# Optimization experiments

Hardware: AMD Instinct MI355X
Metric: run time of the kernel (lower is better)

The kernel has to match this reference:

```python
import jax, jax.numpy as jnp
import numpy as np

EPS = 1e-5

def _conv3x3(x, w, b):
    y = jax.lax.conv_general_dilated(x, w, window_strides=(1, 1),
                                     padding=((1, 1), (1, 1)),
                                     dimension_numbers=('NCHW', 'OIHW', 'NCHW'))
    return y + b[None, :, None, None]

def _bilinear_gather(x, py, px):
    # x: [B,C,H,W]; py,px: [B,K,H,W] absolute sampling coords; zero outside image (DCN convention).
    B, C, H, W = x.shape
    Kk = py.shape[1]
    y0 = jnp.floor(py)
    x0 = jnp.floor(px)
    ly = py - y0
    lx = px - x0
    y0i = y0.astype(jnp.int32)
    x0i = x0.astype(jnp.int32)
    xf = x.reshape(B, C, H * W)

    def gather(yi, xi):
        valid = (yi >= 0) & (yi < H) & (xi >= 0) & (xi < W)
        idx = (jnp.clip(yi, 0, H - 1) * W + jnp.clip(xi, 0, W - 1)).reshape(B, -1)
        g = jax.vmap(lambda xb, ib: xb[:, ib])(xf, idx).reshape(B, C, Kk, H, W)
        return g * valid[:, None].astype(x.dtype)

    v00 = gather(y0i, x0i)
    v01 = gather(y0i, x0i + 1)
    v10 = gather(y0i + 1, x0i)
    v11 = gather(y0i + 1, x0i + 1)
    ly = ly[:, None]
    lx = lx[:, None]
    return (v00 * (1 - ly) * (1 - lx) + v01 * (1 - ly) * lx
            + v10 * ly * (1 - lx) + v11 * ly * lx)

def _shift_forward(x, w_off, b_off, w_conv, b_conv, gamma, beta, run_mean, run_var):
    B, C, H, W = x.shape
    om = _conv3x3(x, w_off, b_off)              # [B,27,H,W] offset/mask predictor
    dy = om[:, 0:18:2]                          # [B,9,H,W] per-tap y offsets
    dx = om[:, 1:18:2]                          # [B,9,H,W] per-tap x offsets
    mask = jax.nn.sigmoid(om[:, 18:27])         # [B,9,H,W] modulation (DCNv2)
    kk = jnp.arange(3, dtype=x.dtype) - 1.0     # kernel tap offsets for 3x3, dilation 1
    ky = jnp.repeat(kk, 3)                      # [9]
    kx = jnp.tile(kk, 3)                        # [9]
    hh = jnp.arange(H, dtype=x.dtype)
    ww = jnp.arange(W, dtype=x.dtype)
    py = hh[None, None, :, None] + ky[None, :, None, None] + dy
    px = ww[None, None, None, :] + kx[None, :, None, None] + dx
    s = _bilinear_gather(x, py, px) * mask[:, None]   # [B,C,9,H,W]
    Co = w_conv.shape[0]
    y = jnp.einsum('bckhw,ock->bohw', s, w_conv.reshape(Co, C, 9))
    y = y + b_conv[None, :, None, None]
    # BatchNorm2d (inference) + ReLU, then residual add
    inv = jax.lax.rsqrt(run_var + EPS)
    y = (y - run_mean[None, :, None, None]) * (inv * gamma)[None, :, None, None] + beta[None, :, None, None]
    y = jax.nn.relu(y)
    return x + y

def setup_inputs():
    key = jax.random.key(0)
    ks = jax.random.split(key, 3)
    B, C, H, W = 2, 256, 96, 96
    x = jax.random.normal(ks[0], (B, C, H, W), dtype=jnp.float32)
    w_off = jax.random.normal(ks[1], (27, C, 3, 3), dtype=jnp.float32) * 0.01
    b_off = jnp.zeros((27,), dtype=jnp.float32)
    w_conv = jax.random.normal(ks[2], (C, C, 3, 3), dtype=jnp.float32) * 0.02
    b_conv = jnp.zeros((C,), dtype=jnp.float32)
    gamma = jnp.ones((C,), dtype=jnp.float32)
    beta = jnp.zeros((C,), dtype=jnp.float32)
    run_mean = jnp.zeros((C,), dtype=jnp.float32)
    run_var = jnp.ones((C,), dtype=jnp.float32)
    return {"x": x, "w_off": w_off, "b_off": b_off, "w_conv": w_conv,
            "b_conv": b_conv, "gamma": gamma, "beta": beta,
            "run_mean": run_mean, "run_var": run_var}

def reference(x, w_off, b_off, w_conv, b_conv, gamma, beta, run_mean, run_var):
    return _shift_forward(x, w_off, b_off, w_conv, b_conv, gamma, beta, run_mean, run_var)
```

## Files before the change

kernel.cpp:

```cpp
#include <hip/hip_runtime.h>
#include <hip/hip_bf16.h>

#define H_ 96
#define W_ 96
#define HW_ 9216
#define C_ 256
#define B_ 2
#define KO_ 27
#define NPX_ 18432
#define EPS_ 1e-5f

typedef unsigned short u16;
typedef unsigned short ushort8 __attribute__((ext_vector_type(8)));
typedef unsigned short ushort4v __attribute__((ext_vector_type(4)));
typedef short short8v __attribute__((ext_vector_type(8)));
typedef float float4v __attribute__((ext_vector_type(4)));

__device__ __forceinline__ float b2f(u16 u) {
    return __uint_as_float(((unsigned int)u) << 16);
}
__device__ __forceinline__ u16 f2b(float f) {
    __hip_bfloat16 h = __float2bfloat16(f);
    union { __hip_bfloat16 h; u16 u; } cv; cv.h = h; return cv.u;
}
__device__ __forceinline__ unsigned int pack2(float a, float b) {
    union { __hip_bfloat162 h; unsigned int u; } cv;
    cv.h = __float22bfloat162_rn(make_float2(a, b));
    return cv.u;
}

__global__ __launch_bounds__(256) void prep_kernel(
    const float* __restrict__ x,
    const float* __restrict__ w_conv, const float* __restrict__ w_off,
    const float* __restrict__ b_conv,
    const float* __restrict__ gamma, const float* __restrict__ beta,
    const float* __restrict__ rmean, const float* __restrict__ rvar,
    float* __restrict__ AB, u16* __restrict__ WQ, u16* __restrict__ WO,
    u16* __restrict__ XT)
{
    __shared__ u16 ls[32][100];
    const int bx = blockIdx.x;
    if (bx < 2304) {
        if (bx == 0) {
            int o = threadIdx.x;
            float sc = gamma[o] * rsqrtf(rvar[o] + EPS_);
            AB[o] = sc;
            AB[256 + o] = beta[o] + (b_conv[o] - rmean[o]) * sc;
        }
        int idx = bx * 256 + threadIdx.x;
        int ch = idx >> 13;
        int o  = (idx >> 5) & 255;
        int cp = idx & 31;
        int c  = ((ch & 7) << 5) + cp;
        int k  = ch >> 3;
        WQ[idx] = f2b(w_conv[(o * C_ + c) * 9 + k]);
    } else if (bx < 2592) {
        int j = (bx - 2304) * 256 + threadIdx.x;
        int ch = j >> 10;
        int o  = (j >> 5) & 31;
        int cp = j & 31;
        int c  = ((ch & 7) << 5) + cp;
        int k  = ch >> 3;
        WO[j] = (o < KO_) ? f2b(w_off[(o * C_ + c) * 9 + k]) : (u16)0;
    } else {
        int bid = bx - 2592;
        int h  = bid % 96;
        int by = bid / 96;
        int cg = by & 7;
        int b  = by >> 3;
        int c0 = cg * 32;
        for (int e = threadIdx.x; e < 32 * W_; e += 256) {
            int ci = e / W_, w = e % W_;
            ls[ci][w] = f2b(x[((b * C_ + c0 + ci) * H_ + h) * W_ + w]);
        }
        __syncthreads();
        for (int u = threadIdx.x; u < 768; u += 256) {
            int g4 = u & 7, w = u >> 3;
            ushort4v v;
#pragma unroll
            for (int t = 0; t < 4; t++) v[t] = ls[g4 * 4 + t][w];
            *(ushort4v*)&XT[((b * H_ + h) * W_ + w) * C_ + c0 + g4 * 4] = v;
        }
    }
}

__global__ __launch_bounds__(256) void fused_kernel(
    const float* __restrict__ x, const u16* __restrict__ XT,
    const u16* __restrict__ WO, const float* __restrict__ b_off,
    const u16* __restrict__ WQ, const float* __restrict__ AB,
    float* __restrict__ out)
{
    __shared__ float red[4][2][32][17];
    __shared__ __align__(16) u16 sB[2048];
    __shared__ float offv[32][36];

    const int tid  = threadIdx.x;
    const int wave = tid >> 6;
    const int lane = tid & 63;
    const int quad = lane >> 4;
    const int l15  = lane & 15;

    const int bid = blockIdx.x;
    const int swz = (bid & 7) * 72 + (bid >> 3);
    const int n0  = swz * 32;
    const int b   = n0 / HW_;
    const int p0  = n0 - b * HW_;
    const int h   = p0 / W_;
    const int w0  = p0 % W_;

    {
        float4v oa[2][2];
#pragma unroll
        for (int ph = 0; ph < 2; ph++)
#pragma unroll
            for (int hh = 0; hh < 2; hh++)
                oa[ph][hh] = float4v{0.f, 0.f, 0.f, 0.f};

        int basec0 = 0, basec1 = 0; bool vld0 = true, vld1 = true;
        auto oset = [&](int tap) {
            int py = h + tap / 3 - 1;
            bool vy = (unsigned)py < (unsigned)H_;
            int pyc = min(max(py, 0), H_ - 1);
            int rowb = (b * H_ + pyc) * W_;
            {
                int pxl = w0 + l15 + tap % 3 - 1;
                vld0 = vy && ((unsigned)pxl < (unsigned)W_);
                basec0 = (rowb + min(max(pxl, 0), W_ - 1)) * C_ + quad * 8;
            }
            {
                int pxl = w0 + 16 + l15 + tap % 3 - 1;
                vld1 = vy && ((unsigned)pxl < (unsigned)W_);
                basec1 = (rowb + min(max(pxl, 0), W_ - 1)) * C_ + quad * 8;
            }
        };
        auto bld0 = [&](int c32) -> ushort8 {
            ushort8 v = *(const ushort8*)(XT + basec0 + (c32 & 7) * 32);
#pragma unroll
            for (int j = 0; j < 8; j++) v[j] = vld0 ? v[j] : (u16)0;
            return v;
        };
        auto bld1 = [&](int c32) -> ushort8 {
            ushort8 v = *(const ushort8*)(XT + basec1 + (c32 & 7) * 32);
#pragma unroll
            for (int j = 0; j < 8; j++) v[j] = vld1 ? v[j] : (u16)0;
            return v;
        };
        const int i0 = wave * 18, i1 = i0 + 18;
        int curtap = i0 >> 3;
        oset(curtap);
        ushort8 b0 = bld0(i0), b1 = bld1(i0);
        short8v wa = *(const short8v*)(WO + i0 * 1024 + l15 * 32 + quad * 8);
        short8v wb = *(const short8v*)(WO + i0 * 1024 + l15 * 32 + quad * 8 + 512);
        for (int i = i0; i < i1; ++i) {
            ushort8 c0v = b0, c1v = b1;
            short8v wac = wa, wbc = wb;
            int nx = i + 1;
            if (nx < i1) {
                int t = nx >> 3;
                if (t != curtap) { oset(t); curtap = t; }
                b0 = bld0(nx); b1 = bld1(nx);
                wa = *(const short8v*)(WO + nx * 1024 + l15 * 32 + quad * 8);
                wb = *(const short8v*)(WO + nx * 1024 + l15 * 32 + quad * 8 + 512);
            }
            union { ushort8 u; short8v s; } u0, u1; u0.u = c0v; u1.u = c1v;
            oa[0][0] = __builtin_amdgcn_mfma_f32_16x16x32_bf16(wac, u0.s, oa[0][0], 0, 0, 0);
            oa[0][1] = __builtin_amdgcn_mfma_f32_16x16x32_bf16(wbc, u0.s, oa[0][1], 0, 0, 0);
            oa[1][0] = __builtin_amdgcn_mfma_f32_16x16x32_bf16(wac, u1.s, oa[1][0], 0, 0, 0);
            oa[1][1] = __builtin_amdgcn_mfma_f32_16x16x32_bf16(wbc, u1.s, oa[1][1], 0, 0, 0);
        }
#pragma unroll
        for (int r = 0; r < 4; ++r) {
            red[wave][0][quad * 4 + r][l15]      = oa[0][0][r];
            red[wave][0][16 + quad * 4 + r][l15] = oa[0][1][r];
            red[wave][1][quad * 4 + r][l15]      = oa[1][0][r];
            red[wave][1][16 + quad * 4 + r][l15] = oa[1][1][r];
        }
    }
    __syncthreads();
    for (int u = tid; u < 1024; u += 256) {
        int px = u & 31, o = u >> 5;
        if (o < KO_) {
            int ph = px >> 4, pp = px & 15;
            float v = red[0][ph][o][pp] + red[1][ph][o][pp]
                    + red[2][ph][o][pp] + red[3][ph][o][pp] + b_off[o];
            offv[px][o] = (o < 18) ? v : 1.f / (1.f + expf(-v));
        }
    }
    __syncthreads();

    float4v acc[4][2];
#pragma unroll
    for (int i = 0; i < 4; i++)
#pragma unroll
        for (int jj = 0; jj < 2; jj++)
            acc[i][jj] = float4v{0.f, 0.f, 0.f, 0.f};

    const int wo  = wave * 64;
    const int ppx = tid >> 3;
    const int pj  = tid & 7;
    const int sboff = (pj >> 2) * 1024 + ppx * 32 + (((pj & 3) ^ (ppx & 3)) << 3);
    const int bslot = (quad ^ (l15 & 3)) << 3;

    float fc0, fc1, fc2, fc3, fn0, fn1, fn2, fn3;
    int a00, a01, a10, a11;

    auto tap_setup = [&](int tap) {
        float dy = offv[ppx][2 * tap];
        float dx = offv[ppx][2 * tap + 1];
        float m  = offv[ppx][18 + tap];
        float py  = (float)(h + tap / 3 - 1) + dy;
        float pxx = (float)(w0 + ppx + tap % 3 - 1) + dx;
        float y0f = floorf(py), x0f = floorf(pxx);
        float ly = py - y0f, lx = pxx - x0f;
        int y0 = (int)y0f, x0i = (int)x0f;
        int y1 = y0 + 1, x1 = x0i + 1;
        bool vy0 = (unsigned)y0 < (unsigned)H_;
        bool vy1 = (unsigned)y1 < (unsigned)H_;
        bool vx0 = (unsigned)x0i < (unsigned)W_;
        bool vx1 = (unsigned)x1 < (unsigned)W_;
        fn0 = (vy0 && vx0) ? (1.f - ly) * (1.f - lx) * m : 0.f;
        fn1 = (vy0 && vx1) ? (1.f - ly) * lx * m : 0.f;
        fn2 = (vy1 && vx0) ? ly * (1.f - lx) * m : 0.f;
        fn3 = (vy1 && vx1) ? ly * lx * m : 0.f;
        int y0c = min(max(y0, 0), H_ - 1), y1c = min(max(y1, 0), H_ - 1);
        int x0c = min(max(x0i, 0), W_ - 1), x1c = min(max(x1, 0), W_ - 1);
        a00 = ((b * H_ + y0c) * W_ + x0c) * C_;
        a01 = ((b * H_ + y0c) * W_ + x1c) * C_;
        a10 = ((b * H_ + y1c) * W_ + x0c) * C_;
        a11 = ((b * H_ + y1c) * W_ + x1c) * C_;
    };

    tap_setup(0);
    fc0 = fn0; fc1 = fn1; fc2 = fn2; fc3 = fn3;
    ushort8 gc00 = *(const ushort8*)(XT + a00 + pj * 8);
    ushort8 gc01 = *(const ushort8*)(XT + a01 + pj * 8);
    ushort8 gc10 = *(const ushort8*)(XT + a10 + pj * 8);
    ushort8 gc11 = *(const ushort8*)(XT + a11 + pj * 8);
    ushort8 gn00{}, gn01{}, gn10{}, gn11{};

#pragma unroll 1
    for (int ch = 0; ch < 36; ++ch) {
        const int tap = ch >> 2, q = ch & 3;

        short8v af[2][4];
        const u16* wq0 = WQ + (size_t)(tap * 8 + q * 2) * 8192
                       + (wo + l15) * 32 + quad * 8;
#pragma unroll
        for (int cc = 0; cc < 2; ++cc)
#pragma unroll
            for (int mt = 0; mt < 4; ++mt)
                af[cc][mt] = *(const short8v*)(wq0 + cc * 8192 + mt * 512);

        {
            float v[8];
#pragma unroll
            for (int t = 0; t < 8; t++)
                v[t] = fc0 * b2f(gc00[t]) + fc1 * b2f(gc01[t])
                     + fc2 * b2f(gc10[t]) + fc3 * b2f(gc11[t]);
            uint4 sv;
            sv.x = pack2(v[0], v[1]);
            sv.y = pack2(v[2], v[3]);
            sv.z = pack2(v[4], v[5]);
            sv.w = pack2(v[6], v[7]);
            *(uint4*)&sB[sboff] = sv;
        }

        if (ch < 35) {
            const int chn = ch + 1, tapn = chn >> 2, qn = chn & 3;
            if (qn == 0) tap_setup(tapn);
            const int cb = qn * 64 + pj * 8;
            gn00 = *(const ushort8*)(XT + a00 + cb);
            gn01 = *(const ushort8*)(XT + a01 + cb);
            gn10 = *(const ushort8*)(XT + a10 + cb);
            gn11 = *(const ushort8*)(XT + a11 + cb);
        }

        asm volatile("s_waitcnt lgkmcnt(0)" ::: "memory");
        __builtin_amdgcn_s_barrier();

        short8v bfr[2][2];
#pragma unroll
        for (int cc = 0; cc < 2; ++cc)
#pragma unroll
            for (int nt = 0; nt < 2; ++nt)
                bfr[cc][nt] = *(const short8v*)
                    &sB[cc * 1024 + (nt * 16 + l15) * 32 + bslot];

        asm volatile("s_waitcnt lgkmcnt(0)" ::: "memory");
        __builtin_amdgcn_s_barrier();
        __builtin_amdgcn_sched_barrier(0);

        __builtin_amdgcn_s_setprio(1);
#pragma unroll
        for (int cc = 0; cc < 2; ++cc)
#pragma unroll
            for (int mt = 0; mt < 4; ++mt)
#pragma unroll
                for (int nt = 0; nt < 2; ++nt)
                    acc[mt][nt] = __builtin_amdgcn_mfma_f32_16x16x32_bf16(
                        af[cc][mt], bfr[cc][nt], acc[mt][nt], 0, 0, 0);
        __builtin_amdgcn_s_setprio(0);

        gc00 = gn00; gc01 = gn01; gc10 = gn10; gc11 = gn11;
        fc0 = fn0; fc1 = fn1; fc2 = fn2; fc3 = fn3;
    }

    const float* Ao = AB;
    const float* Bo = AB + 256;
#pragma unroll
    for (int mt = 0; mt < 4; mt++) {
#pragma unroll
        for (int nt = 0; nt < 2; nt++) {
            int pix = p0 + nt * 16 + l15;
#pragma unroll
            for (int r = 0; r < 4; r++) {
                int o = wo + mt * 16 + quad * 4 + r;
                float v = acc[mt][nt][r] * Ao[o] + Bo[o];
                v = fmaxf(v, 0.f);
                int gi = (b * C_ + o) * HW_ + pix;
                out[gi] = x[gi] + v;
            }
        }
    }
}

extern "C" void kernel_launch(void* const* d_in, const int* in_sizes, int n_in,
                              void* d_out, int out_size, void* d_ws, size_t ws_size,
                              hipStream_t stream)
{
    (void)in_sizes; (void)n_in; (void)out_size; (void)ws_size;
    const float* x      = (const float*)d_in[0];
    const float* w_off  = (const float*)d_in[1];
    const float* b_off  = (const float*)d_in[2];
    const float* w_conv = (const float*)d_in[3];
    const float* b_conv = (const float*)d_in[4];
    const float* gamma  = (const float*)d_in[5];
    const float* beta   = (const float*)d_in[6];
    const float* rmean  = (const float*)d_in[7];
    const float* rvar   = (const float*)d_in[8];
    float* out = (float*)d_out;

    float* ws = (float*)d_ws;
    float* AB = ws;
    u16* WQ = (u16*)(AB + 512);
    u16* WO = WQ + 589824;
    u16* XT = WO + 73728;

    prep_kernel<<<4128, 256, 0, stream>>>(x, w_conv, w_off, b_conv, gamma, beta,
                                          rmean, rvar, AB, WQ, WO, XT);
    fused_kernel<<<576, 256, 0, stream>>>(x, XT, WO, b_off, WQ, AB, out);
}
```

Baseline: 175.0 us.

## Split output channels across two blocks and stage weights via async LDS loads

Each block now computes 128 output channels for its 32 pixels, so the grid grows to 1152 blocks. The A-side weight tiles are double-buffered in LDS with global_load_lds, and the prep kernel stores them in a swizzled layout so the LDS reads avoid bank conflicts. The sampled B tile is also double-buffered, with XT prefetched two chunks ahead. The aim is better occupancy across the CUs and less stall on per-wave global weight loads. In exchange, each output-channel half recomputes the offset conv and the bilinear sampling, and the kernel uses more LDS per block.

Measured after the change: 184.7 us. +5.6%, slower.

```diff
diff --git a/kernel.cpp b/kernel.cpp
--- a/kernel.cpp
+++ b/kernel.cpp
@@ -5,9 +5,7 @@
 #define W_ 96
 #define HW_ 9216
 #define C_ 256
-#define B_ 2
 #define KO_ 27
-#define NPX_ 18432
 #define EPS_ 1e-5f
 
 typedef unsigned short u16;
@@ -27,6 +25,11 @@
     union { __hip_bfloat162 h; unsigned int u; } cv;
     cv.h = __float22bfloat162_rn(make_float2(a, b));
     return cv.u;
+}
+__device__ __forceinline__ void glds16(const u16* g, u16* l) {
+    __builtin_amdgcn_global_load_lds(
+        (const __attribute__((address_space(1))) void*)g,
+        (__attribute__((address_space(3))) void*)l, 16, 0, 0);
 }
 
 __global__ __launch_bounds__(256) void prep_kernel(
@@ -50,7 +53,8 @@
         int idx = bx * 256 + threadIdx.x;
         int ch = idx >> 13;
         int o  = (idx >> 5) & 255;
-        int cp = idx & 31;
+        int cpa = idx & 31;
+        int cp  = cpa ^ ((o & 3) << 3);
         int c  = ((ch & 7) << 5) + cp;
         int k  = ch >> 3;
         WQ[idx] = f2b(w_conv[(o * C_ + c) * 9 + k]);
@@ -90,19 +94,23 @@
     const u16* __restrict__ WQ, const float* __restrict__ AB,
     float* __restrict__ out)
 {
-    __shared__ float red[4][2][32][17];
-    __shared__ __align__(16) u16 sB[2048];
-    __shared__ float offv[32][36];
+    __shared__ __align__(16) unsigned char smem[45568];
+    u16*   sA   = (u16*)smem;
+    u16*   sB   = (u16*)(smem + 32768);
+    float* offv = (float*)(smem + 40960);
+    float (*red)[2][32][17] = (float (*)[2][32][17])smem;
 
     const int tid  = threadIdx.x;
     const int wave = tid >> 6;
     const int lane = tid & 63;
     const int quad = lane >> 4;
     const int l15  = lane & 15;
+    const int qx   = (quad ^ (l15 & 3)) << 3;
 
     const int bid = blockIdx.x;
-    const int swz = (bid & 7) * 72 + (bid >> 3);
-    const int n0  = swz * 32;
+    const int swz = (bid & 7) * 144 + (bid >> 3);
+    const int o0  = (swz & 1) << 7;
+    const int n0  = (swz >> 1) * 32;
     const int b   = n0 / HW_;
     const int p0  = n0 - b * HW_;
     const int h   = p0 / W_;
@@ -183,31 +191,31 @@
             int ph = px >> 4, pp = px & 15;
             float v = red[0][ph][o][pp] + red[1][ph][o][pp]
                     + red[2][ph][o][pp] + red[3][ph][o][pp] + b_off[o];
-            offv[px][o] = (o < 18) ? v : 1.f / (1.f + expf(-v));
+            offv[px * 36 + o] = (o < 18) ? v : 1.f / (1.f + expf(-v));
         }
     }
     __syncthreads();
 
-    float4v acc[4][2];
-#pragma unroll
-    for (int i = 0; i < 4; i++)
+    float4v acc[2][2];
+#pragma unroll
+    for (int i = 0; i < 2; i++)
 #pragma unroll
         for (int jj = 0; jj < 2; jj++)
             acc[i][jj] = float4v{0.f, 0.f, 0.f, 0.f};
 
-    const int wo  = wave * 64;
+    const int le8 = lane * 8;
+    const int wo  = wave * 32;
     const int ppx = tid >> 3;
     const int pj  = tid & 7;
-    const int sboff = (pj >> 2) * 1024 + ppx * 32 + (((pj & 3) ^ (ppx & 3)) << 3);
-    const int bslot = (quad ^ (l15 & 3)) << 3;
+    const int sbw = (pj >> 2) * 1024 + ppx * 32 + (((pj & 3) ^ (ppx & 3)) << 3);
 
     float fc0, fc1, fc2, fc3, fn0, fn1, fn2, fn3;
     int a00, a01, a10, a11;
 
     auto tap_setup = [&](int tap) {
-        float dy = offv[ppx][2 * tap];
-        float dx = offv[ppx][2 * tap + 1];
-        float m  = offv[ppx][18 + tap];
+        float dy = offv[ppx * 36 + 2 * tap];
+        float dx = offv[ppx * 36 + 2 * tap + 1];
+        float m  = offv[ppx * 36 + 18 + tap];
         float py  = (float)(h + tap / 3 - 1) + dy;
         float pxx = (float)(w0 + ppx + tap % 3 - 1) + dx;
         float y0f = floorf(py), x0f = floorf(pxx);
@@ -229,28 +237,71 @@
         a10 = ((b * H_ + y1c) * W_ + x0c) * C_;
         a11 = ((b * H_ + y1c) * W_ + x1c) * C_;
     };
+    auto stageA = [&](int chn, int buf) {
+#pragma unroll
+        for (int i = 0; i < 4; ++i) {
+            int unit = i * 4 + wave;
+            int cc = unit >> 3;
+            glds16(WQ + (size_t)(chn * 2 + cc) * 8192 + o0 * 32
+                      + (unit & 7) * 512 + le8,
+                   sA + buf * 8192 + unit * 512);
+        }
+    };
 
     tap_setup(0);
     fc0 = fn0; fc1 = fn1; fc2 = fn2; fc3 = fn3;
-    ushort8 gc00 = *(const ushort8*)(XT + a00 + pj * 8);
-    ushort8 gc01 = *(const ushort8*)(XT + a01 + pj * 8);
-    ushort8 gc10 = *(const ushort8*)(XT + a10 + pj * 8);
-    ushort8 gc11 = *(const ushort8*)(XT + a11 + pj * 8);
-    ushort8 gn00{}, gn01{}, gn10{}, gn11{};
+    ushort8 t00 = *(const ushort8*)(XT + a00 + pj * 8);
+    ushort8 t01 = *(const ushort8*)(XT + a01 + pj * 8);
+    ushort8 t10 = *(const ushort8*)(XT + a10 + pj * 8);
+    ushort8 t11 = *(const ushort8*)(XT + a11 + pj * 8);
+    stageA(0, 0);
+    ushort8 gc00 = *(const ushort8*)(XT + a00 + 64 + pj * 8);
+    ushort8 gc01 = *(const ushort8*)(XT + a01 + 64 + pj * 8);
+    ushort8 gc10 = *(const ushort8*)(XT + a10 + 64 + pj * 8);
+    ushort8 gc11 = *(const ushort8*)(XT + a11 + 64 + pj * 8);
+    {
+        float v[8];
+#pragma unroll
+        for (int t = 0; t < 8; t++)
+            v[t] = fc0 * b2f(t00[t]) + fc1 * b2f(t01[t])
+                 + fc2 * b2f(t10[t]) + fc3 * b2f(t11[t]);
+        uint4 sv;
+        sv.x = pack2(v[0], v[1]); sv.y = pack2(v[2], v[3]);
+        sv.z = pack2(v[4], v[5]); sv.w = pack2(v[6], v[7]);
+        *(uint4*)&sB[sbw] = sv;
+    }
+    asm volatile("s_waitcnt lgkmcnt(0)" ::: "memory");
+    __builtin_amdgcn_s_barrier();
 
 #pragma unroll 1
-    for (int ch = 0; ch < 36; ++ch) {
-        const int tap = ch >> 2, q = ch & 3;
-
-        short8v af[2][4];
-        const u16* wq0 = WQ + (size_t)(tap * 8 + q * 2) * 8192
-                       + (wo + l15) * 32 + quad * 8;
-#pragma unroll
-        for (int cc = 0; cc < 2; ++cc)
-#pragma unroll
-            for (int mt = 0; mt < 4; ++mt)
-                af[cc][mt] = *(const short8v*)(wq0 + cc * 8192 + mt * 512);
-
+    for (int ch = 0; ch < 35; ++ch) {
+        const int p = ch & 1;
+        stageA(ch + 1, p ^ 1);
+        ushort8 gn00{}, gn01{}, gn10{}, gn11{};
+        if (ch <= 33) {
+            const int c2 = ch + 2;
+            if ((c2 & 3) == 0) tap_setup(c2 >> 2);
+            const int cb = (c2 & 3) * 64 + pj * 8;
+            gn00 = *(const ushort8*)(XT + a00 + cb);
+            gn01 = *(const ushort8*)(XT + a01 + cb);
+            gn10 = *(const ushort8*)(XT + a10 + cb);
+            gn11 = *(const ushort8*)(XT + a11 + cb);
+        }
+        asm volatile("s_waitcnt vmcnt(8)" ::: "memory");
+        __builtin_amdgcn_sched_barrier(0);
+
+        short8v af[2][2], bfr[2][2];
+#pragma unroll
+        for (int cc = 0; cc < 2; ++cc) {
+#pragma unroll
+            for (int mt = 0; mt < 2; ++mt)
+                af[cc][mt] = *(const short8v*)
+                    &sA[p * 8192 + cc * 4096 + (wo + mt * 16 + l15) * 32 + qx];
+#pragma unroll
+            for (int nt = 0; nt < 2; ++nt)
+                bfr[cc][nt] = *(const short8v*)
+                    &sB[p * 2048 + cc * 1024 + (nt * 16 + l15) * 32 + qx];
+        }
         {
             float v[8];
 #pragma unroll
@@ -258,33 +309,12 @@
                 v[t] = fc0 * b2f(gc00[t]) + fc1 * b2f(gc01[t])
                      + fc2 * b2f(gc10[t]) + fc3 * b2f(gc11[t]);
             uint4 sv;
-            sv.x = pack2(v[0], v[1]);
-            sv.y = pack2(v[2], v[3]);
-            sv.z = pack2(v[4], v[5]);
-            sv.w = pack2(v[6], v[7]);
-            *(uint4*)&sB[sboff] = sv;
-        }
-
-        if (ch < 35) {
-            const int chn = ch + 1, tapn = chn >> 2, qn = chn & 3;
-            if (qn == 0) tap_setup(tapn);
-            const int cb = qn * 64 + pj * 8;
-            gn00 = *(const ushort8*)(XT + a00 + cb);
-            gn01 = *(const ushort8*)(XT + a01 + cb);
-            gn10 = *(const ushort8*)(XT + a10 + cb);
-            gn11 = *(const ushort8*)(XT + a11 + cb);
-        }
-
-        asm volatile("s_waitcnt lgkmcnt(0)" ::: "memory");
-        __builtin_amdgcn_s_barrier();
-
-        short8v bfr[2][2];
-#pragma unroll
-        for (int cc = 0; cc < 2; ++cc)
-#pragma unroll
-            for (int nt = 0; nt < 2; ++nt)
-                bfr[cc][nt] = *(const short8v*)
-                    &sB[cc * 1024 + (nt * 16 + l15) * 32 + bslot];
+            sv.x = pack2(v[0], v[1]); sv.y = pack2(v[2], v[3]);
+            sv.z = pack2(v[4], v[5]); sv.w = pack2(v[6], v[7]);
+            *(uint4*)&sB[(p ^ 1) * 2048 + sbw] = sv;
+        }
+        if (ch <= 33) { gc00 = gn00; gc01 = gn01; gc10 = gn10; gc11 = gn11; }
+        if (((ch + 2) & 3) == 0) { fc0 = fn0; fc1 = fn1; fc2 = fn2; fc3 = fn3; }
 
         asm volatile("s_waitcnt lgkmcnt(0)" ::: "memory");
         __builtin_amdgcn_s_barrier();
@@ -294,27 +324,50 @@
 #pragma unroll
         for (int cc = 0; cc < 2; ++cc)
 #pragma unroll
-            for (int mt = 0; mt < 4; ++mt)
+            for (int mt = 0; mt < 2; ++mt)
 #pragma unroll
                 for (int nt = 0; nt < 2; ++nt)
                     acc[mt][nt] = __builtin_amdgcn_mfma_f32_16x16x32_bf16(
                         af[cc][mt], bfr[cc][nt], acc[mt][nt], 0, 0, 0);
         __builtin_amdgcn_s_setprio(0);
-
-        gc00 = gn00; gc01 = gn01; gc10 = gn10; gc11 = gn11;
-        fc0 = fn0; fc1 = fn1; fc2 = fn2; fc3 = fn3;
+    }
+    {
+        asm volatile("s_waitcnt vmcnt(0)" ::: "memory");
+        __builtin_amdgcn_sched_barrier(0);
+        short8v af[2][2], bfr[2][2];
+#pragma unroll
+        for (int cc = 0; cc < 2; ++cc) {
+#pragma unroll
+            for (int mt = 0; mt < 2; ++mt)
+                af[cc][mt] = *(const short8v*)
+                    &sA[8192 + cc * 4096 + (wo + mt * 16 + l15) * 32 + qx];
+#pragma unroll
+            for (int nt = 0; nt < 2; ++nt)
+                bfr[cc][nt] = *(const short8v*)
+                    &sB[2048 + cc * 1024 + (nt * 16 + l15) * 32 + qx];
+        }
+        asm volatile("s_waitcnt lgkmcnt(0)" ::: "memory");
+        __builtin_amdgcn_sched_barrier(0);
+#pragma unroll
+        for (int cc = 0; cc < 2; ++cc)
+#pragma unroll
+            for (int mt = 0; mt < 2; ++mt)
+#pragma unroll
+                for (int nt = 0; nt < 2; ++nt)
+                    acc[mt][nt] = __builtin_amdgcn_mfma_f32_16x16x32_bf16(
+                        af[cc][mt], bfr[cc][nt], acc[mt][nt], 0, 0, 0);
     }
 
     const float* Ao = AB;
     const float* Bo = AB + 256;
 #pragma unroll
-    for (int mt = 0; mt < 4; mt++) {
+    for (int mt = 0; mt < 2; mt++) {
 #pragma unroll
         for (int nt = 0; nt < 2; nt++) {
             int pix = p0 + nt * 16 + l15;
 #pragma unroll
             for (int r = 0; r < 4; r++) {
-                int o = wo + mt * 16 + quad * 4 + r;
+                int o = o0 + wo + mt * 16 + quad * 4 + r;
                 float v = acc[mt][nt][r] * Ao[o] + Bo[o];
                 v = fmaxf(v, 0.f);
                 int gi = (b * C_ + o) * HW_ + pix;
@@ -348,5 +401,5 @@
 
     prep_kernel<<<4128, 256, 0, stream>>>(x, w_conv, w_off, b_conv, gamma, beta,
                                           rmean, rvar, AB, WQ, WO, XT);
-    fused_kernel<<<576, 256, 0, stream>>>(x, XT, WO, b_off, WQ, AB, out);
-}
+    fused_kernel<<<1152, 256, 0, stream>>>(x, XT, WO, b_off, WQ, AB, out);
+}
```

## Split offset conv into separate kernel, halve output channels per block, stage weights via LDS

Applied to the files above, without the earlier changes.

The offset/mask predictor moves out of the fused kernel into its own kernel that writes offsets to a workspace buffer. The main kernel now covers 128 output channels per block, doubling the grid to 1152 blocks. Its weight tiles are staged into LDS with global_load_lds instead of being read directly from global memory into registers. The prep kernel is reorganised so weight transposes go through LDS per output channel and fewer blocks are launched. This aims to improve occupancy and load balance, at the cost of an extra launch, an offsets round-trip through memory, and recomputing the bilinear sampling once per channel half.

Result: slower. 195.3 us (+11.6%).

```diff
diff --git a/kernel.cpp b/kernel.cpp
--- a/kernel.cpp
+++ b/kernel.cpp
@@ -5,9 +5,7 @@
 #define W_ 96
 #define HW_ 9216
 #define C_ 256
-#define B_ 2
 #define KO_ 27
-#define NPX_ 18432
 #define EPS_ 1e-5f
 
 typedef unsigned short u16;
@@ -27,6 +25,11 @@
     union { __hip_bfloat162 h; unsigned int u; } cv;
     cv.h = __float22bfloat162_rn(make_float2(a, b));
     return cv.u;
+}
+__device__ __forceinline__ void glds16(const u16* g, u16* l) {
+    __builtin_amdgcn_global_load_lds(
+        (const __attribute__((address_space(1))) void*)g,
+        (__attribute__((address_space(3))) void*)l, 16, 0, 0);
 }
 
 __global__ __launch_bounds__(256) void prep_kernel(
@@ -38,61 +41,63 @@
     float* __restrict__ AB, u16* __restrict__ WQ, u16* __restrict__ WO,
     u16* __restrict__ XT)
 {
-    __shared__ u16 ls[32][100];
+    __shared__ u16 sbuf[3200];
     const int bx = blockIdx.x;
-    if (bx < 2304) {
-        if (bx == 0) {
-            int o = threadIdx.x;
-            float sc = gamma[o] * rsqrtf(rvar[o] + EPS_);
-            AB[o] = sc;
-            AB[256 + o] = beta[o] + (b_conv[o] - rmean[o]) * sc;
-        }
-        int idx = bx * 256 + threadIdx.x;
-        int ch = idx >> 13;
-        int o  = (idx >> 5) & 255;
-        int cp = idx & 31;
-        int c  = ((ch & 7) << 5) + cp;
-        int k  = ch >> 3;
-        WQ[idx] = f2b(w_conv[(o * C_ + c) * 9 + k]);
-    } else if (bx < 2592) {
-        int j = (bx - 2304) * 256 + threadIdx.x;
-        int ch = j >> 10;
-        int o  = (j >> 5) & 31;
-        int cp = j & 31;
-        int c  = ((ch & 7) << 5) + cp;
-        int k  = ch >> 3;
-        WO[j] = (o < KO_) ? f2b(w_off[(o * C_ + c) * 9 + k]) : (u16)0;
+    const int tid = threadIdx.x;
+
+    if (bx < 384) {
+        u16 (*ls)[100] = (u16 (*)[100])sbuf;
+        int h    = bx % 96;
+        int t2   = bx / 96;
+        int b    = t2 >> 1;
+        int half = t2 & 1;
+        for (int cgi = 0; cgi < 4; ++cgi) {
+            int c0 = (half * 4 + cgi) * 32;
+            for (int e = tid; e < 32 * W_; e += 256) {
+                int ci = e / W_, w = e % W_;
+                ls[ci][w] = f2b(x[((b * C_ + c0 + ci) * H_ + h) * W_ + w]);
+            }
+            __syncthreads();
+            for (int u = tid; u < 768; u += 256) {
+                int g4 = u & 7, w = u >> 3;
+                ushort4v v;
+#pragma unroll
+                for (int t = 0; t < 4; t++) v[t] = ls[g4 * 4 + t][w];
+                *(ushort4v*)&XT[((b * H_ + h) * W_ + w) * C_ + c0 + g4 * 4] = v;
+            }
+            __syncthreads();
+        }
+    } else if (bx < 640) {
+        int o = bx - 384;
+        for (int i = tid; i < 2304; i += 256)
+            sbuf[i] = f2b(w_conv[o * 2304 + i]);
+        __syncthreads();
+        int cg = tid >> 5, ln = tid & 31;
+#pragma unroll
+        for (int k = 0; k < 9; ++k)
+            WQ[(k * 8 + cg) * 8192 + o * 32 + ln] = sbuf[(cg * 32 + ln) * 9 + k];
+    } else if (bx < 672) {
+        int o = bx - 640;
+        for (int i = tid; i < 2304; i += 256)
+            sbuf[i] = (o < KO_) ? f2b(w_off[o * 2304 + i]) : (u16)0;
+        __syncthreads();
+        int cg = tid >> 5, ln = tid & 31;
+#pragma unroll
+        for (int k = 0; k < 9; ++k)
+            WO[(k * 8 + cg) * 1024 + o * 32 + ln] = sbuf[(cg * 32 + ln) * 9 + k];
     } else {
-        int bid = bx - 2592;
-        int h  = bid % 96;
-        int by = bid / 96;
-        int cg = by & 7;
-        int b  = by >> 3;
-        int c0 = cg * 32;
-        for (int e = threadIdx.x; e < 32 * W_; e += 256) {
-            int ci = e / W_, w = e % W_;
-            ls[ci][w] = f2b(x[((b * C_ + c0 + ci) * H_ + h) * W_ + w]);
-        }
-        __syncthreads();
-        for (int u = threadIdx.x; u < 768; u += 256) {
-            int g4 = u & 7, w = u >> 3;
-            ushort4v v;
-#pragma unroll
-            for (int t = 0; t < 4; t++) v[t] = ls[g4 * 4 + t][w];
-            *(ushort4v*)&XT[((b * H_ + h) * W_ + w) * C_ + c0 + g4 * 4] = v;
-        }
-    }
-}
-
-__global__ __launch_bounds__(256) void fused_kernel(
-    const float* __restrict__ x, const u16* __restrict__ XT,
-    const u16* __restrict__ WO, const float* __restrict__ b_off,
-    const u16* __restrict__ WQ, const float* __restrict__ AB,
-    float* __restrict__ out)
+        int o = tid;
+        float sc = gamma[o] * rsqrtf(rvar[o] + EPS_);
+        AB[o] = sc;
+        AB[256 + o] = beta[o] + (b_conv[o] - rmean[o]) * sc;
+    }
+}
+
+__global__ __launch_bounds__(256) void offsets_kernel(
+    const u16* __restrict__ XT, const u16* __restrict__ WO,
+    const float* __restrict__ b_off, float* __restrict__ OFF)
 {
     __shared__ float red[4][2][32][17];
-    __shared__ __align__(16) u16 sB[2048];
-    __shared__ float offv[32][36];
 
     const int tid  = threadIdx.x;
     const int wave = tid >> 6;
@@ -100,81 +105,77 @@
     const int quad = lane >> 4;
     const int l15  = lane & 15;
 
-    const int bid = blockIdx.x;
-    const int swz = (bid & 7) * 72 + (bid >> 3);
-    const int n0  = swz * 32;
-    const int b   = n0 / HW_;
-    const int p0  = n0 - b * HW_;
-    const int h   = p0 / W_;
-    const int w0  = p0 % W_;
-
-    {
-        float4v oa[2][2];
-#pragma unroll
-        for (int ph = 0; ph < 2; ph++)
-#pragma unroll
-            for (int hh = 0; hh < 2; hh++)
-                oa[ph][hh] = float4v{0.f, 0.f, 0.f, 0.f};
-
-        int basec0 = 0, basec1 = 0; bool vld0 = true, vld1 = true;
-        auto oset = [&](int tap) {
-            int py = h + tap / 3 - 1;
-            bool vy = (unsigned)py < (unsigned)H_;
-            int pyc = min(max(py, 0), H_ - 1);
-            int rowb = (b * H_ + pyc) * W_;
-            {
-                int pxl = w0 + l15 + tap % 3 - 1;
-                vld0 = vy && ((unsigned)pxl < (unsigned)W_);
-                basec0 = (rowb + min(max(pxl, 0), W_ - 1)) * C_ + quad * 8;
-            }
-            {
-                int pxl = w0 + 16 + l15 + tap % 3 - 1;
-                vld1 = vy && ((unsigned)pxl < (unsigned)W_);
-                basec1 = (rowb + min(max(pxl, 0), W_ - 1)) * C_ + quad * 8;
-            }
-        };
-        auto bld0 = [&](int c32) -> ushort8 {
-            ushort8 v = *(const ushort8*)(XT + basec0 + (c32 & 7) * 32);
-#pragma unroll
-            for (int j = 0; j < 8; j++) v[j] = vld0 ? v[j] : (u16)0;
-            return v;
-        };
-        auto bld1 = [&](int c32) -> ushort8 {
-            ushort8 v = *(const ushort8*)(XT + basec1 + (c32 & 7) * 32);
-#pragma unroll
-            for (int j = 0; j < 8; j++) v[j] = vld1 ? v[j] : (u16)0;
-            return v;
-        };
-        const int i0 = wave * 18, i1 = i0 + 18;
-        int curtap = i0 >> 3;
-        oset(curtap);
-        ushort8 b0 = bld0(i0), b1 = bld1(i0);
-        short8v wa = *(const short8v*)(WO + i0 * 1024 + l15 * 32 + quad * 8);
-        short8v wb = *(const short8v*)(WO + i0 * 1024 + l15 * 32 + quad * 8 + 512);
-        for (int i = i0; i < i1; ++i) {
-            ushort8 c0v = b0, c1v = b1;
-            short8v wac = wa, wbc = wb;
-            int nx = i + 1;
-            if (nx < i1) {
-                int t = nx >> 3;
-                if (t != curtap) { oset(t); curtap = t; }
-                b0 = bld0(nx); b1 = bld1(nx);
-                wa = *(const short8v*)(WO + nx * 1024 + l15 * 32 + quad * 8);
-                wb = *(const short8v*)(WO + nx * 1024 + l15 * 32 + quad * 8 + 512);
-            }
-            union { ushort8 u; short8v s; } u0, u1; u0.u = c0v; u1.u = c1v;
-            oa[0][0] = __builtin_amdgcn_mfma_f32_16x16x32_bf16(wac, u0.s, oa[0][0], 0, 0, 0);
-            oa[0][1] = __builtin_amdgcn_mfma_f32_16x16x32_bf16(wbc, u0.s, oa[0][1], 0, 0, 0);
-            oa[1][0] = __builtin_amdgcn_mfma_f32_16x16x32_bf16(wac, u1.s, oa[1][0], 0, 0, 0);
-            oa[1][1] = __builtin_amdgcn_mfma_f32_16x16x32_bf16(wbc, u1.s, oa[1][1], 0, 0, 0);
-        }
-#pragma unroll
-        for (int r = 0; r < 4; ++r) {
-            red[wave][0][quad * 4 + r][l15]      = oa[0][0][r];
-            red[wave][0][16 + quad * 4 + r][l15] = oa[0][1][r];
-            red[wave][1][quad * 4 + r][l15]      = oa[1][0][r];
-            red[wave][1][16 + quad * 4 + r][l15] = oa[1][1][r];
-        }
+    const int n0 = blockIdx.x * 32;
+    const int b  = n0 / HW_;
+    const int p0 = n0 - b * HW_;
+    const int h  = p0 / W_;
+    const int w0 = p0 % W_;
+
+    float4v oa[2][2];
+#pragma unroll
+    for (int ph = 0; ph < 2; ph++)
+#pragma unroll
+        for (int hh = 0; hh < 2; hh++)
+            oa[ph][hh] = float4v{0.f, 0.f, 0.f, 0.f};
+
+    int basec0 = 0, basec1 = 0; bool vld0 = true, vld1 = true;
+    auto oset = [&](int tap) {
+        int py = h + tap / 3 - 1;
+        bool vy = (unsigned)py < (unsigned)H_;
+        int pyc = min(max(py, 0), H_ - 1);
+        int rowb = (b * H_ + pyc) * W_;
+        {
+            int pxl = w0 + l15 + tap % 3 - 1;
+            vld0 = vy && ((unsigned)pxl < (unsigned)W_);
+            basec0 = (rowb + min(max(pxl, 0), W_ - 1)) * C_ + quad * 8;
+        }
+        {
+            int pxl = w0 + 16 + l15 + tap % 3 - 1;
+            vld1 = vy && ((unsigned)pxl < (unsigned)W_);
+            basec1 = (rowb + min(max(pxl, 0), W_ - 1)) * C_ + quad * 8;
+        }
+    };
+    auto bld0 = [&](int c32) -> ushort8 {
+        ushort8 v = *(const ushort8*)(XT + basec0 + (c32 & 7) * 32);
+#pragma unroll
+        for (int j = 0; j < 8; j++) v[j] = vld0 ? v[j] : (u16)0;
+        return v;
+    };
+    auto bld1 = [&](int c32) -> ushort8 {
+        ushort8 v = *(const ushort8*)(XT + basec1 + (c32 & 7) * 32);
+#pragma unroll
+        for (int j = 0; j < 8; j++) v[j] = vld1 ? v[j] : (u16)0;
+        return v;
+    };
+    const int i0 = wave * 18, i1 = i0 + 18;
+    int curtap = i0 >> 3;
+    oset(curtap);
+    ushort8 b0 = bld0(i0), b1 = bld1(i0);
+    short8v wa = *(const short8v*)(WO + i0 * 1024 + l15 * 32 + quad * 8);
+    short8v wb = *(const short8v*)(WO + i0 * 1024 + l15 * 32 + quad * 8 + 512);
+    for (int i = i0; i < i1; ++i) {
+        ushort8 c0v = b0, c1v = b1;
+        short8v wac = wa, wbc = wb;
+        int nx = i + 1;
+        if (nx < i1) {
+            int t = nx >> 3;
+            if (t != curtap) { oset(t); curtap = t; }
+            b0 = bld0(nx); b1 = bld1(nx);
+            wa = *(const short8v*)(WO + nx * 1024 + l15 * 32 + quad * 8);
+            wb = *(const short8v*)(WO + nx * 1024 + l15 * 32 + quad * 8 + 512);
+        }
+        union { ushort8 u; short8v s; } u0, u1; u0.u = c0v; u1.u = c1v;
+        oa[0][0] = __builtin_amdgcn_mfma_f32_16x16x32_bf16(wac, u0.s, oa[0][0], 0, 0, 0);
+        oa[0][1] = __builtin_amdgcn_mfma_f32_16x16x32_bf16(wbc, u0.s, oa[0][1], 0, 0, 0);
+        oa[1][0] = __builtin_amdgcn_mfma_f32_16x16x32_bf16(wac, u1.s, oa[1][0], 0, 0, 0);
+        oa[1][1] = __builtin_amdgcn_mfma_f32_16x16x32_bf16(wbc, u1.s, oa[1][1], 0, 0, 0);
+    }
+#pragma unroll
+    for (int r = 0; r < 4; ++r) {
+        red[wave][0][quad * 4 + r][l15]      = oa[0][0][r];
+        red[wave][0][16 + quad * 4 + r][l15] = oa[0][1][r];
+        red[wave][1][quad * 4 + r][l15]      = oa[1][0][r];
+        red[wave][1][16 + quad * 4 + r][l15] = oa[1][1][r];
     }
     __syncthreads();
     for (int u = tid; u < 1024; u += 256) {
@@ -183,23 +184,56 @@
             int ph = px >> 4, pp = px & 15;
             float v = red[0][ph][o][pp] + red[1][ph][o][pp]
                     + red[2][ph][o][pp] + red[3][ph][o][pp] + b_off[o];
-            offv[px][o] = (o < 18) ? v : 1.f / (1.f + expf(-v));
-        }
+            OFF[(size_t)(n0 + px) * 32 + o] =
+                (o < 18) ? v : 1.f / (1.f + expf(-v));
+        }
+    }
+}
+
+__global__ __launch_bounds__(256) void fused_kernel(
+    const float* __restrict__ x, const u16* __restrict__ XT,
+    const float* __restrict__ OFF, const u16* __restrict__ WQ,
+    const float* __restrict__ AB, float* __restrict__ out)
+{
+    __shared__ __align__(16) u16 sA[8192];
+    __shared__ __align__(16) u16 sB[2048];
+    __shared__ float offv[32][32];
+
+    const int tid  = threadIdx.x;
+    const int wave = tid >> 6;
+    const int lane = tid & 63;
+    const int quad = lane >> 4;
+    const int l15  = lane & 15;
+
+    const int bid = blockIdx.x;
+    const int swz = (bid & 7) * 144 + (bid >> 3);
+    const int o0  = (swz & 1) << 7;
+    const int n0  = (swz >> 1) * 32;
+    const int b   = n0 / HW_;
+    const int p0  = n0 - b * HW_;
+    const int h   = p0 / W_;
+    const int w0  = p0 % W_;
+
+    {
+        int px = tid >> 3, q4 = (tid & 7) * 4;
+        float4 v = *(const float4*)(OFF + (size_t)(n0 + px) * 32 + q4);
+        *(float4*)&offv[px][q4] = v;
     }
     __syncthreads();
 
-    float4v acc[4][2];
-#pragma unroll
-    for (int i = 0; i < 4; i++)
+    float4v acc[2][2];
+#pragma unroll
+    for (int i = 0; i < 2; i++)
 #pragma unroll
         for (int jj = 0; jj < 2; jj++)
             acc[i][jj] = float4v{0.f, 0.f, 0.f, 0.f};
 
-    const int wo  = wave * 64;
+    const int le8 = lane * 8;
+    const int wo  = wave * 32;
+
     const int ppx = tid >> 3;
     const int pj  = tid & 7;
-    const int sboff = (pj >> 2) * 1024 + ppx * 32 + (((pj & 3) ^ (ppx & 3)) << 3);
-    const int bslot = (quad ^ (l15 & 3)) << 3;
+    const int sboff = (pj >> 2) * 1024 + ppx * 32 + (pj & 3) * 8;
 
     float fc0, fc1, fc2, fc3, fn0, fn1, fn2, fn3;
     int a00, a01, a10, a11;
@@ -229,6 +263,16 @@
         a10 = ((b * H_ + y1c) * W_ + x0c) * C_;
         a11 = ((b * H_ + y1c) * W_ + x1c) * C_;
     };
+    auto stageA = [&](int tap, int q) {
+#pragma unroll
+        for (int i = 0; i < 4; ++i) {
+            int unit = i * 4 + wave;
+            int cc = unit >> 3;
+            glds16(WQ + (size_t)(tap * 8 + q * 2 + cc) * 8192 + o0 * 32
+                      + (unit & 7) * 512 + le8,
+                   &sA[unit * 512]);
+        }
+    };
 
     tap_setup(0);
     fc0 = fn0; fc1 = fn1; fc2 = fn2; fc3 = fn3;
@@ -236,21 +280,11 @@
     ushort8 gc01 = *(const ushort8*)(XT + a01 + pj * 8);
     ushort8 gc10 = *(const ushort8*)(XT + a10 + pj * 8);
     ushort8 gc11 = *(const ushort8*)(XT + a11 + pj * 8);
+    stageA(0, 0);
     ushort8 gn00{}, gn01{}, gn10{}, gn11{};
 
-#pragma unroll 1
+#pragma unroll 4
     for (int ch = 0; ch < 36; ++ch) {
-        const int tap = ch >> 2, q = ch & 3;
-
-        short8v af[2][4];
-        const u16* wq0 = WQ + (size_t)(tap * 8 + q * 2) * 8192
-                       + (wo + l15) * 32 + quad * 8;
-#pragma unroll
-        for (int cc = 0; cc < 2; ++cc)
-#pragma unroll
-            for (int mt = 0; mt < 4; ++mt)
-                af[cc][mt] = *(const short8v*)(wq0 + cc * 8192 + mt * 512);
-
         {
             float v[8];
 #pragma unroll
@@ -264,6 +298,23 @@
             sv.w = pack2(v[6], v[7]);
             *(uint4*)&sB[sboff] = sv;
         }
+        asm volatile("s_waitcnt vmcnt(0) lgkmcnt(0)" ::: "memory");
+        __builtin_amdgcn_s_barrier();
+
+        short8v af[2][2], bfr[2][2];
+#pragma unroll
+        for (int cc = 0; cc < 2; ++cc) {
+#pragma unroll
+            for (int mt = 0; mt < 2; ++mt)
+                af[cc][mt] = *(const short8v*)
+                    &sA[cc * 4096 + (wo + mt * 16 + l15) * 32 + quad * 8];
+#pragma unroll
+            for (int nt = 0; nt < 2; ++nt)
+                bfr[cc][nt] = *(const short8v*)
+                    &sB[cc * 1024 + (nt * 16 + l15) * 32 + quad * 8];
+        }
+        asm volatile("s_waitcnt lgkmcnt(0)" ::: "memory");
+        __builtin_amdgcn_s_barrier();
 
         if (ch < 35) {
             const int chn = ch + 1, tapn = chn >> 2, qn = chn & 3;
@@ -273,34 +324,18 @@
             gn01 = *(const ushort8*)(XT + a01 + cb);
             gn10 = *(const ushort8*)(XT + a10 + cb);
             gn11 = *(const ushort8*)(XT + a11 + cb);
-        }
-
-        asm volatile("s_waitcnt lgkmcnt(0)" ::: "memory");
-        __builtin_amdgcn_s_barrier();
-
-        short8v bfr[2][2];
+            stageA(tapn, qn);
+        }
+        __builtin_amdgcn_s_setprio(1);
 #pragma unroll
         for (int cc = 0; cc < 2; ++cc)
 #pragma unroll
-            for (int nt = 0; nt < 2; ++nt)
-                bfr[cc][nt] = *(const short8v*)
-                    &sB[cc * 1024 + (nt * 16 + l15) * 32 + bslot];
-
-        asm volatile("s_waitcnt lgkmcnt(0)" ::: "memory");
-        __builtin_amdgcn_s_barrier();
-        __builtin_amdgcn_sched_barrier(0);
-
-        __builtin_amdgcn_s_setprio(1);
-#pragma unroll
-        for (int cc = 0; cc < 2; ++cc)
-#pragma unroll
-            for (int mt = 0; mt < 4; ++mt)
+            for (int mt = 0; mt < 2; ++mt)
 #pragma unroll
                 for (int nt = 0; nt < 2; ++nt)
                     acc[mt][nt] = __builtin_amdgcn_mfma_f32_16x16x32_bf16(
                         af[cc][mt], bfr[cc][nt], acc[mt][nt], 0, 0, 0);
         __builtin_amdgcn_s_setprio(0);
-
         gc00 = gn00; gc01 = gn01; gc10 = gn10; gc11 = gn11;
         fc0 = fn0; fc1 = fn1; fc2 = fn2; fc3 = fn3;
     }
@@ -308,13 +343,13 @@
     const float* Ao = AB;
     const float* Bo = AB + 256;
 #pragma unroll
-    for (int mt = 0; mt < 4; mt++) {
+    for (int mt = 0; mt < 2; mt++) {
 #pragma unroll
         for (int nt = 0; nt < 2; nt++) {
             int pix = p0 + nt * 16 + l15;
 #pragma unroll
             for (int r = 0; r < 4; r++) {
-                int o = wo + mt * 16 + quad * 4 + r;
+                int o = o0 + wo + mt * 16 + quad * 4 + r;
                 float v = acc[mt][nt][r] * Ao[o] + Bo[o];
                 v = fmaxf(v, 0.f);
                 int gi = (b * C_ + o) * HW_ + pix;
@@ -345,8 +380,10 @@
     u16* WQ = (u16*)(AB + 512);
     u16* WO = WQ + 589824;
     u16* XT = WO + 73728;
-
-    prep_kernel<<<4128, 256, 0, stream>>>(x, w_conv, w_off, b_conv, gamma, beta,
-                                          rmean, rvar, AB, WQ, WO, XT);
-    fused_kernel<<<576, 256, 0, stream>>>(x, XT, WO, b_off, WQ, AB, out);
-}
+    float* OFF = (float*)(XT + 4718592);
+
+    prep_kernel<<<673, 256, 0, stream>>>(x, w_conv, w_off, b_conv, gamma, beta,
+                                         rmean, rvar, AB, WQ, WO, XT);
+    offsets_kernel<<<576, 256, 0, stream>>>(XT, WO, b_off, OFF);
+    fused_kernel<<<1152, 256, 0, stream>>>(x, XT, OFF, WQ, AB, out);
+}
```
